# Optimization experiments

Hardware: AMD Instinct MI355X
Metric: run time of the kernel (lower is better)

The kernel has to match this reference:

```python
import jax, jax.numpy as jnp
import numpy as np

N_NODES = 100000
N_EDGES = 1600000
D = 128
N_LAYERS = 3
N_CLASSES = 10
N_GRAPHS = 512
BN_EPS = 1e-5


def setup_inputs() -> dict:
    key = jax.random.key(0)
    ks = jax.random.split(key, 16)
    s = 1.0 / np.sqrt(D)
    x = jax.random.normal(ks[0], (N_NODES, D), dtype=jnp.float32)
    edge_index = jax.random.randint(ks[1], (2, N_EDGES), 0, N_NODES, dtype=jnp.int32)
    batch = jnp.sort(jax.random.randint(ks[2], (N_NODES,), 0, N_GRAPHS, dtype=jnp.int32))
    W1s = jax.random.uniform(ks[3], (N_LAYERS, D, D), jnp.float32, -s, s)
    b1s = jax.random.uniform(ks[4], (N_LAYERS, D), jnp.float32, -s, s)
    W2s = jax.random.uniform(ks[5], (N_LAYERS, D, D), jnp.float32, -s, s)
    b2s = jax.random.uniform(ks[6], (N_LAYERS, D), jnp.float32, -s, s)
    gammas = jnp.ones((N_LAYERS, D), jnp.float32)
    betas = jnp.zeros((N_LAYERS, D), jnp.float32)
    lin1_w = jax.random.uniform(ks[7], (D, D), jnp.float32, -s, s)
    lin1_b = jax.random.uniform(ks[8], (D,), jnp.float32, -s, s)
    lin2_w = jax.random.uniform(ks[9], (D, N_CLASSES), jnp.float32, -s, s)
    lin2_b = jax.random.uniform(ks[10], (N_CLASSES,), jnp.float32, -s, s)
    return dict(x=x, edge_index=edge_index, batch=batch, W1s=W1s, b1s=b1s,
                W2s=W2s, b2s=b2s, gammas=gammas, betas=betas,
                lin1_w=lin1_w, lin1_b=lin1_b, lin2_w=lin2_w, lin2_b=lin2_b)


def _gin_layer(x, src, dst, W1, b1, W2, b2, gamma, beta):
    # scatter-add neighbor aggregation: sum_{j->i} x_j   (eps = 0)
    agg = jax.ops.segment_sum(x[src], dst, num_segments=N_NODES)
    h = x + agg
    h = jax.nn.relu(h @ W1 + b1)
    h = jax.nn.relu(h @ W2 + b2)
    # BatchNorm1d, training-mode batch stats (biased variance)
    mu = jnp.mean(h, axis=0)
    var = jnp.var(h, axis=0)
    return gamma * (h - mu) * jax.lax.rsqrt(var + BN_EPS) + beta


def reference(x, edge_index, batch, W1s, b1s, W2s, b2s, gammas, betas,
              lin1_w, lin1_b, lin2_w, lin2_b):
    src, dst = edge_index[0], edge_index[1]
    for l in range(N_LAYERS):
        x = _gin_layer(x, src, dst, W1s[l], b1s[l], W2s[l], b2s[l], gammas[l], betas[l])
    # global mean pool over graphs
    sums = jax.ops.segment_sum(x, batch, num_segments=N_GRAPHS)
    counts = jax.ops.segment_sum(jnp.ones((x.shape[0],), x.dtype), batch, num_segments=N_GRAPHS)
    pooled = sums / jnp.maximum(counts, 1.0)[:, None]
    h = jax.nn.relu(pooled @ lin1_w + lin1_b)  # dropout = identity (eval)
    return h @ lin2_w + lin2_b
```

## Files before the change

### kernel.cpp

```cpp
#include <hip/hip_runtime.h>
#include <hip/hip_bf16.h>

#define N_NODES 100000
#define N_EDGES 1600000
#define DD 128
#define N_GRAPHS 512
#define BN_EPS 1e-5f
#define NTILES 3125
#define SCAN_B 98
#define RED_B 25
#define PART_N 12500

typedef unsigned int u32;
typedef unsigned char u8;
typedef __bf16 bf16_t;
typedef __bf16 bf16x2 __attribute__((ext_vector_type(2)));
typedef __bf16 bf16x4 __attribute__((ext_vector_type(4)));
typedef __bf16 bf16x8 __attribute__((ext_vector_type(8)));
typedef float f32x4 __attribute__((ext_vector_type(4)));

__device__ __forceinline__ float bflo2f(u32 u) {
    union { u32 i; float f; } x; x.i = u << 16; return x.f;
}
__device__ __forceinline__ float bfhi2f(u32 u) {
    union { u32 i; float f; } x; x.i = u & 0xffff0000u; return x.f;
}
__device__ __forceinline__ u32 pack4u(float v0, float v1, float v2, float v3, float inv) {
    u32 q0 = (u32)fminf(rintf(v0 * inv), 255.f);
    u32 q1 = (u32)fminf(rintf(v1 * inv), 255.f);
    u32 q2 = (u32)fminf(rintf(v2 * inv), 255.f);
    u32 q3 = (u32)fminf(rintf(v3 * inv), 255.f);
    return q0 | (q1 << 8) | (q2 << 16) | (q3 << 24);
}


__global__ void k_zero(float4* p, int n) {
    float4 z = make_float4(0.f, 0.f, 0.f, 0.f);
    for (int i = blockIdx.x * blockDim.x + threadIdx.x; i < n; i += gridDim.x * blockDim.x)
        p[i] = z;
}

__global__ void k_hist8(const int* __restrict__ dst, int* __restrict__ deg) {
    const int part = blockIdx.x & 7;
    const int lo = part * PART_N, hi = lo + PART_N;
    const int start = (blockIdx.x >> 3) * blockDim.x + threadIdx.x;
    const int stride = (gridDim.x >> 3) * blockDim.x;
    for (int e = start; e < N_EDGES; e += stride) {
        int d = dst[e];
        if (d >= lo && d < hi) atomicAdd(&deg[d], 1);
    }
}

__global__ void k_scan1(const int* __restrict__ deg, int* __restrict__ bsum) {
    __shared__ int sh[1024];
    int b = blockIdx.x, t = threadIdx.x;
    int i = b * 1024 + t;
    int pd = (i < N_NODES) ? ((deg[i] + 3) & ~3) : 0;
    sh[t] = pd;
    __syncthreads();
    for (int s = 512; s > 0; s >>= 1) {
        if (t < s) sh[t] += sh[t + s];
        __syncthreads();
    }
    if (t == 0) bsum[b] = sh[0];
}
__global__ void k_scan2(const int* __restrict__ bsum, int* __restrict__ bbase,
                        int* __restrict__ poffs) {
    __shared__ int sh[128];
    int t = threadIdx.x;
    int v = (t < SCAN_B) ? bsum[t] : 0;
    sh[t] = v;
    __syncthreads();
    for (int d = 1; d < 128; d <<= 1) {
        int o = (t >= d) ? sh[t - d] : 0;
        __syncthreads();
        sh[t] += o;
        __syncthreads();
    }
    if (t < SCAN_B) bbase[t] = sh[t] - v;
    if (t == SCAN_B - 1) poffs[N_NODES] = sh[t];
}
__global__ void k_scan3(const int* __restrict__ deg, const int* __restrict__ bbase,
                        int* __restrict__ poffs, int* __restrict__ cursor) {
    __shared__ int sh[1024];
    int b = blockIdx.x, t = threadIdx.x;
    int i = b * 1024 + t;
    int pd = (i < N_NODES) ? ((deg[i] + 3) & ~3) : 0;
    sh[t] = pd;
    __syncthreads();
    for (int d = 1; d < 1024; d <<= 1) {
        int o = (t >= d) ? sh[t - d] : 0;
        __syncthreads();
        sh[t] += o;
        __syncthreads();
    }
    if (i < N_NODES) {
        int off = bbase[b] + sh[t] - pd;
        poffs[i] = off; cursor[i] = off;
    }
}

__global__ void k_fill8(const int* __restrict__ src, const int* __restrict__ dst,
                        int* __restrict__ cursor, int* __restrict__ csr) {
    const int part = blockIdx.x & 7;
    const int lo = part * PART_N, hi = lo + PART_N;
    const int start = (blockIdx.x >> 3) * blockDim.x + threadIdx.x;
    const int stride = (gridDim.x >> 3) * blockDim.x;
    for (int e = start; e < N_EDGES; e += stride) {
        int d = dst[e];
        if (d >= lo && d < hi) {
            int pos = atomicAdd(&cursor[d], 1);
            csr[pos] = src[e];
        }
    }
}

__global__ void k_pad(const int* __restrict__ deg, const int* __restrict__ poffs,
                      int* __restrict__ csr) {
    int t = blockIdx.x * blockDim.x + threadIdx.x;
    if (t >= N_NODES * 4) return;
    int n = t >> 2, j = t & 3;
    int s = poffs[n] + deg[n];
    if (s + j < poffs[n + 1]) csr[s + j] = n;
}

__global__ void k_cvt(const float* __restrict__ x, bf16_t* __restrict__ xb) {
    const int n4 = N_NODES * DD / 4;
    const float4* x4 = (const float4*)x;
    bf16x4* o4 = (bf16x4*)xb;
    for (int i = blockIdx.x * blockDim.x + threadIdx.x; i < n4; i += gridDim.x * blockDim.x) {
        float4 v = x4[i];
        bf16x4 o;
        o.x = (bf16_t)v.x; o.y = (bf16_t)v.y; o.z = (bf16_t)v.z; o.w = (bf16_t)v.w;
        o4[i] = o;
    }
}

__global__ void k_shufw(const float* __restrict__ W1s, const float* __restrict__ W2s,
                        bf16_t* __restrict__ wshuf) {
    int t = blockIdx.x * blockDim.x + threadIdx.x;
    if (t >= 6 * 16384) return;
    int g  = t >> 14;
    int r  = t & 16383;
    int j  = r & 7;
    int L  = (r >> 3) & 63;
    int nt = (r >> 9) & 7;
    int ks = r >> 12;
    int l  = g >> 1;
    const float* src = (g & 1) ? (W2s + l * 16384) : (W1s + l * 16384);
    int k = ks * 32 + (L >> 4) * 8 + j;
    int n = nt * 16 + (L & 15);
    wshuf[t] = (bf16_t)src[k * DD + n];
}

__global__ void k_aff_init(float* __restrict__ ss) {
    int f = threadIdx.x;
    if (f < DD) { ss[f] = 1.0f; ss[DD + f] = 0.0f; }
}

__global__ void k_red(const float* __restrict__ pstats, float* __restrict__ red) {
    int b = blockIdx.x;
    int t = threadIdx.x;
    const float* p = pstats + (size_t)b * 125 * 256 + t;
    float acc = 0.f;
    for (int i = 0; i < 125; ++i) acc += p[i * 256];
    red[b * 256 + t] = acc;
}

__global__ void k_aff_update(const float* __restrict__ red, const float* __restrict__ gamma,
                             const float* __restrict__ beta, float* __restrict__ scale,
                             float* __restrict__ shift) {
    int f = threadIdx.x;
    if (f < DD) {
        float s = 0.f, q = 0.f;
        for (int i = 0; i < RED_B; ++i) {
            s += red[i * 256 + f];
            q += red[i * 256 + 128 + f];
        }
        float mu  = s * (1.0f / N_NODES);
        float var = q * (1.0f / N_NODES) - mu * mu;
        float inv = rsqrtf(var + BN_EPS);
        float sc  = gamma[f] * inv;
        scale[f] = sc;
        shift[f] = beta[f] - mu * sc;
    }
}

__global__ void k_gbounds(const int* __restrict__ batch, int* __restrict__ gstart) {
    int i = blockIdx.x * blockDim.x + threadIdx.x;
    if (i >= N_NODES) return;
    int b = batch[i];
    int bp = (i == 0) ? -1 : batch[i - 1];
    for (int g = bp + 1; g <= b; ++g) gstart[g] = i;
    if (i == N_NODES - 1)
        for (int g = b + 1; g <= N_GRAPHS; ++g) gstart[g] = N_NODES;
}


template<bool IN_U8>
__device__ __forceinline__ void load_row8(
    const u8* __restrict__ xg, int r, int l16, float (&v)[8])
{
    if (IN_U8) {
        uint2 d = *(const uint2*)(xg + ((size_t)r << 7) + (l16 << 3));
        v[0] = (float)(d.x & 0xffu);
        v[1] = (float)((d.x >> 8) & 0xffu);
        v[2] = (float)((d.x >> 16) & 0xffu);
        v[3] = (float)(d.x >> 24);
        v[4] = (float)(d.y & 0xffu);
        v[5] = (float)((d.y >> 8) & 0xffu);
        v[6] = (float)((d.y >> 16) & 0xffu);
        v[7] = (float)(d.y >> 24);
    } else {
        uint4 d = *(const uint4*)(xg + ((size_t)r << 8) + (l16 << 4));
        v[0] = bflo2f(d.x); v[1] = bfhi2f(d.x);
        v[2] = bflo2f(d.y); v[3] = bfhi2f(d.y);
        v[4] = bflo2f(d.z); v[5] = bfhi2f(d.z);
        v[6] = bflo2f(d.w); v[7] = bfhi2f(d.w);
    }
}

template<bool IN_U8>
__device__ __forceinline__ void acc_group(
    const u8* __restrict__ xg, const float* __restrict__ xsc,
    int r, int l16, float (&a)[8])
{
    float v[8];
    load_row8<IN_U8>(xg, r, l16, v);
    if (IN_U8) {
        float s = xsc[r];
#pragma unroll
        for (int j = 0; j < 8; ++j) a[j] += s * v[j];
    } else {
#pragma unroll
        for (int j = 0; j < 8; ++j) a[j] += v[j];
    }
}

template<bool IN_U8>
__global__ __launch_bounds__(128, 8) void k_gather(
    const bf16_t* __restrict__ xb,
    const u8* __restrict__ x8, const float* __restrict__ xsc,
    const int* __restrict__ poffs, const int* __restrict__ csr,
    const int* __restrict__ deg,
    const float* __restrict__ scale, const float* __restrict__ shift,
    bf16_t* __restrict__ xt)
{
    const int tid  = threadIdx.x;
    const int w    = tid >> 6;
    const int lane = tid & 63;
    const int base = blockIdx.x * 32;
    const int q4   = lane >> 4;
    const int l16  = lane & 15;

    const u8* xg = IN_U8 ? x8 : (const u8*)xb;

    for (int rp = 0; rp < 8; ++rp) {
        const int rowA = (w << 4) + rp;
        const int rowB = rowA + 8;
        const int nA = base + rowA;
        const int nB = base + rowB;

        float aA[8] = {0.f, 0.f, 0.f, 0.f, 0.f, 0.f, 0.f, 0.f};
        float aB[8] = {0.f, 0.f, 0.f, 0.f, 0.f, 0.f, 0.f, 0.f};

        int eA = poffs[nA], eEA = poffs[nA + 1];
        int eB = poffs[nB], eEB = poffs[nB + 1];

        int rA = csr[eA + q4];
        int rB = csr[eB + q4];

        while ((eA < eEA) & (eB < eEB)) {
            int rA2 = csr[eA + 4 + q4];
            int rB2 = csr[eB + 4 + q4];
            acc_group<IN_U8>(xg, xsc, rA, l16, aA);
            acc_group<IN_U8>(xg, xsc, rB, l16, aB);
            rA = rA2; rB = rB2; eA += 4; eB += 4;
        }
        while (eA < eEA) {
            acc_group<IN_U8>(xg, xsc, rA, l16, aA);
            eA += 4; rA = csr[eA + q4];
        }
        while (eB < eEB) {
            acc_group<IN_U8>(xg, xsc, rB, l16, aB);
            eB += 4; rB = csr[eB + q4];
        }

        const int dgA = deg[nA], dgB = deg[nB];
        const float scoA = 1.f - (float)(((dgA + 3) & ~3) - dgA);
        const float scoB = 1.f - (float)(((dgB + 3) & ~3) - dgB);
        {
            int rs = (q4 & 1) ? nB : nA;
            float v[8];
            load_row8<IN_U8>(xg, rs, l16, v);
            float coA = (q4 == 0) ? scoA : 0.f;
            float coB = (q4 == 1) ? scoB : 0.f;
            if (IN_U8) {
                float s = xsc[rs];
                coA *= s; coB *= s;
            }
#pragma unroll
            for (int j = 0; j < 8; ++j) {
                aA[j] += coA * v[j];
                aB[j] += coB * v[j];
            }
        }

#pragma unroll
        for (int j = 0; j < 8; ++j) {
            aA[j] += __shfl_xor(aA[j], 16);
            aA[j] += __shfl_xor(aA[j], 32);
            aB[j] += __shfl_xor(aB[j], 16);
            aB[j] += __shfl_xor(aB[j], 32);
        }

        if (q4 < 2) {
            const bool selA = (q4 == 0);
            const float4 s0 = *(const float4*)(scale + (l16 << 3));
            const float4 s1 = *(const float4*)(scale + (l16 << 3) + 4);
            const float4 t0 = *(const float4*)(shift + (l16 << 3));
            const float4 t1 = *(const float4*)(shift + (l16 << 3) + 4);
            const float sarr[8] = {s0.x, s0.y, s0.z, s0.w, s1.x, s1.y, s1.z, s1.w};
            const float tarr[8] = {t0.x, t0.y, t0.z, t0.w, t1.x, t1.y, t1.z, t1.w};
            const int   node = selA ? nA : nB;
            const float cnt = (float)((selA ? dgA : dgB) + 1);
            bf16x8 pk;
#pragma unroll
            for (int j = 0; j < 8; ++j) {
                float av = selA ? aA[j] : aB[j];
                pk[j] = (bf16_t)(av * sarr[j] + cnt * tarr[j]);
            }
            *(bf16x8*)(xt + (size_t)node * DD + (l16 << 3)) = pk;
        }
    }
}

__global__ __launch_bounds__(128, 8) void k_mlp(
    const bf16_t* __restrict__ xt,
    u8* __restrict__ y8, float* __restrict__ ysc,
    const bf16_t* __restrict__ w1s, const bf16_t* __restrict__ w2s,
    const float* __restrict__ b1, const float* __restrict__ b2,
    float* __restrict__ pstats)
{
    __shared__ __align__(16) bf16_t tile[32 * 136];
    __shared__ float swsum[2][128];
    __shared__ float swsq[2][128];

    const int tid  = threadIdx.x;
    const int w    = tid >> 6;
    const int lane = tid & 63;
    const int base = blockIdx.x * 32;

    const int q = lane >> 4;
    const int c16 = lane & 15;
    const int arow = (w << 4) + c16;

    bf16x8 afr[4];
#pragma unroll
    for (int ks = 0; ks < 4; ++ks)
        afr[ks] = *(const bf16x8*)(xt + (size_t)(base + arow) * DD + ks * 32 + q * 8);

    f32x4 acc[8];
#pragma unroll
    for (int nt = 0; nt < 8; ++nt) acc[nt] = (f32x4){0.f, 0.f, 0.f, 0.f};
#pragma unroll
    for (int ks = 0; ks < 4; ++ks) {
#pragma unroll
        for (int nt = 0; nt < 8; ++nt) {
            bf16x8 bfr = *(const bf16x8*)(w1s + (((ks << 3) + nt) * 64 + lane) * 8);
            acc[nt] = __builtin_amdgcn_mfma_f32_16x16x32_bf16(afr[ks], bfr, acc[nt], 0, 0, 0);
        }
    }
#pragma unroll
    for (int nt = 0; nt < 8; ++nt) {
        float bias = b1[(nt << 4) + c16];
#pragma unroll
        for (int i = 0; i < 4; ++i) {
            float v = fmaxf(acc[nt][i] + bias, 0.f);
            int row = (w << 4) + (q << 2) + i;
            tile[row * 136 + (nt << 4) + c16] = (bf16_t)v;
        }
    }
    __syncthreads();

    bf16x8 afr2[4];
#pragma unroll
    for (int ks = 0; ks < 4; ++ks)
        afr2[ks] = *(const bf16x8*)(&tile[arow * 136 + ks * 32 + q * 8]);
    __syncthreads();

#pragma unroll
    for (int nt = 0; nt < 8; ++nt) acc[nt] = (f32x4){0.f, 0.f, 0.f, 0.f};
#pragma unroll
    for (int ks = 0; ks < 4; ++ks) {
#pragma unroll
        for (int nt = 0; nt < 8; ++nt) {
            bf16x8 bfr = *(const bf16x8*)(w2s + (((ks << 3) + nt) * 64 + lane) * 8);
            acc[nt] = __builtin_amdgcn_mfma_f32_16x16x32_bf16(afr2[ks], bfr, acc[nt], 0, 0, 0);
        }
    }
#pragma unroll
    for (int nt = 0; nt < 8; ++nt) {
        float bias = b2[(nt << 4) + c16];
        float s1 = 0.f, s2 = 0.f;
#pragma unroll
        for (int i = 0; i < 4; ++i) {
            float v = fmaxf(acc[nt][i] + bias, 0.f);
            int row = (w << 4) + (q << 2) + i;
            s1 += v;
            s2 += v * v;
            tile[row * 136 + (nt << 4) + c16] = (bf16_t)v;
        }
        s1 += __shfl_down(s1, 32); s2 += __shfl_down(s2, 32);
        s1 += __shfl_down(s1, 16); s2 += __shfl_down(s2, 16);
        if (lane < 16) {
            swsum[w][(nt << 4) + lane] = s1;
            swsq[w][(nt << 4) + lane] = s2;
        }
    }
    __syncthreads();

    {
        float ps = swsum[0][tid & 127] + swsum[1][tid & 127];
        float pq = swsq[0][tid & 127] + swsq[1][tid & 127];
        float* pb = pstats + (size_t)blockIdx.x * 256;
        pb[tid] = ps;
        pb[128 + tid] = pq;
    }

    {
        int row4 = tid >> 2, t4 = tid & 3;
        int node = base + row4;
        const bf16_t* tp = tile + row4 * 136 + t4 * 32;
        bf16x8 v0 = *(const bf16x8*)(tp);
        bf16x8 v1 = *(const bf16x8*)(tp + 8);
        bf16x8 v2 = *(const bf16x8*)(tp + 16);
        bf16x8 v3 = *(const bf16x8*)(tp + 24);
        float am = 0.f;
#pragma unroll
        for (int k = 0; k < 8; ++k) {
            am = fmaxf(am, (float)v0[k]);
            am = fmaxf(am, (float)v1[k]);
            am = fmaxf(am, (float)v2[k]);
            am = fmaxf(am, (float)v3[k]);
        }
        am = fmaxf(am, __shfl_xor(am, 1));
        am = fmaxf(am, __shfl_xor(am, 2));
        float inv = am > 0.f ? 255.f / am : 0.f;
        if (t4 == 0) ysc[node] = am * (1.f / 255.f);
        u32 u[8];
        u[0] = pack4u((float)v0[0], (float)v0[1], (float)v0[2], (float)v0[3], inv);
        u[1] = pack4u((float)v0[4], (float)v0[5], (float)v0[6], (float)v0[7], inv);
        u[2] = pack4u((float)v1[0], (float)v1[1], (float)v1[2], (float)v1[3], inv);
        u[3] = pack4u((float)v1[4], (float)v1[5], (float)v1[6], (float)v1[7], inv);
        u[4] = pack4u((float)v2[0], (float)v2[1], (float)v2[2], (float)v2[3], inv);
        u[5] = pack4u((float)v2[4], (float)v2[5], (float)v2[6], (float)v2[7], inv);
        u[6] = pack4u((float)v3[0], (float)v3[1], (float)v3[2], (float)v3[3], inv);
        u[7] = pack4u((float)v3[4], (float)v3[5], (float)v3[6], (float)v3[7], inv);
        uint4* yp = (uint4*)(y8 + (size_t)node * DD + t4 * 32);
        yp[0] = make_uint4(u[0], u[1], u[2], u[3]);
        yp[1] = make_uint4(u[4], u[5], u[6], u[7]);
    }
}


__global__ __launch_bounds__(256) void k_pool2u(
    const u8* __restrict__ y8, const float* __restrict__ ysc,
    const int* __restrict__ gstart,
    const float* __restrict__ scale, const float* __restrict__ shift,
    float* __restrict__ pooled)
{
    __shared__ float part[128];
    int g = blockIdx.x;
    int t = threadIdx.x;
    int f = t & 127, h = t >> 7;
    int s = gstart[g], e = gstart[g + 1];
    float acc = 0.f;
    for (int n = s + h; n < e; n += 2)
        acc += ysc[n] * (float)y8[(size_t)n * DD + f];
    if (h == 1) part[f] = acc;
    __syncthreads();
    if (h == 0) {
        acc += part[f];
        float cnt = (float)(e - s);
        float v = acc * scale[f] + cnt * shift[f];
        pooled[g * DD + f] = v / fmaxf(cnt, 1.0f);
    }
}

__global__ void k_head(const float* __restrict__ pooled,
                       const float* __restrict__ lin1w, const float* __restrict__ lin1b,
                       const float* __restrict__ lin2w, const float* __restrict__ lin2b,
                       float* __restrict__ out) {
    __shared__ float p[DD];
    __shared__ float h[DD];
    int g = blockIdx.x;
    int t = threadIdx.x;
    p[t] = pooled[g * DD + t];
    __syncthreads();
    float a = lin1b[t];
    for (int k = 0; k < DD; ++k) a += p[k] * lin1w[k * DD + t];
    h[t] = fmaxf(a, 0.f);
    __syncthreads();
    if (t < 10) {
        float o = lin2b[t];
        for (int k = 0; k < DD; ++k) o += h[k] * lin2w[k * 10 + t];
        out[g * 10 + t] = o;
    }
}


extern "C" void kernel_launch(void* const* d_in, const int* in_sizes, int n_in,
                              void* d_out, int out_size, void* d_ws, size_t ws_size,
                              hipStream_t stream) {
    const float* x      = (const float*)d_in[0];
    const int*   ei     = (const int*)d_in[1];
    const int*   batch  = (const int*)d_in[2];
    const float* W1s    = (const float*)d_in[3];
    const float* b1s    = (const float*)d_in[4];
    const float* W2s    = (const float*)d_in[5];
    const float* b2s    = (const float*)d_in[6];
    const float* gammas = (const float*)d_in[7];
    const float* betas  = (const float*)d_in[8];
    const float* lin1w  = (const float*)d_in[9];
    const float* lin1b  = (const float*)d_in[10];
    const float* lin2w  = (const float*)d_in[11];
    const float* lin2b  = (const float*)d_in[12];
    float* out = (float*)d_out;

    char* p = (char*)d_ws;
    size_t off = 0;
    auto alloc = [&](size_t bytes) -> char* {
        char* r = p + off;
        off += (bytes + 255) & ~(size_t)255;
        return r;
    };
    int*    deg    = (int*)alloc(N_NODES * 4);
    size_t zero_bytes = off;
    int*    poffs  = (int*)alloc((N_NODES + 1) * 4);
    int*    cursor = (int*)alloc(N_NODES * 4);
    int*    bsum   = (int*)alloc(128 * 4);
    int*    bbase  = (int*)alloc(128 * 4);
    int*    csr    = (int*)alloc(((size_t)N_EDGES + 4 * N_NODES + 64) * 4);
    bf16_t* xb     = (bf16_t*)alloc((size_t)N_NODES * DD * 2);
    u8*     q8a    = (u8*)alloc((size_t)N_NODES * DD);
    float*  sca    = (float*)alloc(N_NODES * 4);
    float*  scb    = (float*)alloc(N_NODES * 4);
    bf16_t* wshuf  = (bf16_t*)alloc(6 * 16384 * 2);
    float*  ss     = (float*)alloc(4 * 256 * 4);
    int*    gstart = (int*)alloc((N_GRAPHS + 1) * 4);
    float*  pooled = (float*)alloc(N_GRAPHS * DD * 4);
    bf16_t* xt     = (bf16_t*)alloc((size_t)N_NODES * DD * 2);
    float*  pstats = (float*)alloc((size_t)NTILES * 256 * 4);
    float*  red    = (float*)alloc(RED_B * 256 * 4);
    if (off > ws_size) return;

    u8* q8b = (u8*)xb;

    const int* srcA = ei;
    const int* dstA = ei + N_EDGES;

    k_zero<<<256, 256, 0, stream>>>((float4*)d_ws, (int)(zero_bytes / 16));
    k_hist8<<<1024, 256, 0, stream>>>(dstA, deg);
    k_scan1<<<SCAN_B, 1024, 0, stream>>>(deg, bsum);
    k_scan2<<<1, 128, 0, stream>>>(bsum, bbase, poffs);
    k_scan3<<<SCAN_B, 1024, 0, stream>>>(deg, bbase, poffs, cursor);
    k_fill8<<<1024, 256, 0, stream>>>(srcA, dstA, cursor, csr);
    k_pad<<<(N_NODES * 4 + 255) / 256, 256, 0, stream>>>(deg, poffs, csr);
    k_cvt<<<1024, 256, 0, stream>>>(x, xb);
    k_shufw<<<(6 * 16384 + 255) / 256, 256, 0, stream>>>(W1s, W2s, wshuf);
    k_aff_init<<<1, 128, 0, stream>>>(ss);
    k_gbounds<<<(N_NODES + 255) / 256, 256, 0, stream>>>(batch, gstart);

    k_gather<false><<<NTILES, 128, 0, stream>>>(
        xb, q8a, sca, poffs, csr, deg,
        ss + 0 * 256, ss + 0 * 256 + 128, xt);
    k_mlp<<<NTILES, 128, 0, stream>>>(
        xt, q8a, sca,
        wshuf + 0 * 16384, wshuf + 1 * 16384,
        b1s + 0 * DD, b2s + 0 * DD, pstats);
    k_red<<<RED_B, 256, 0, stream>>>(pstats, red);
    k_aff_update<<<1, 128, 0, stream>>>(red, gammas + 0 * DD, betas + 0 * DD,
                                        ss + 1 * 256, ss + 1 * 256 + 128);

    k_gather<true><<<NTILES, 128, 0, stream>>>(
        xb, q8a, sca, poffs, csr, deg,
        ss + 1 * 256, ss + 1 * 256 + 128, xt);
    k_mlp<<<NTILES, 128, 0, stream>>>(
        xt, q8b, scb,
        wshuf + 2 * 16384, wshuf + 3 * 16384,
        b1s + 1 * DD, b2s + 1 * DD, pstats);
    k_red<<<RED_B, 256, 0, stream>>>(pstats, red);
    k_aff_update<<<1, 128, 0, stream>>>(red, gammas + 1 * DD, betas + 1 * DD,
                                        ss + 2 * 256, ss + 2 * 256 + 128);

    k_gather<true><<<NTILES, 128, 0, stream>>>(
        xb, q8b, scb, poffs, csr, deg,
        ss + 2 * 256, ss + 2 * 256 + 128, xt);
    k_mlp<<<NTILES, 128, 0, stream>>>(
        xt, q8a, sca,
        wshuf + 4 * 16384, wshuf + 5 * 16384,
        b1s + 2 * DD, b2s + 2 * DD, pstats);
    k_red<<<RED_B, 256, 0, stream>>>(pstats, red);
    k_aff_update<<<1, 128, 0, stream>>>(red, gammas + 2 * DD, betas + 2 * DD,
                                        ss + 3 * 256, ss + 3 * 256 + 128);

    k_pool2u<<<N_GRAPHS, 256, 0, stream>>>(q8a, sca, gstart,
                                           ss + 3 * 256, ss + 3 * 256 + 128, pooled);
    k_head<<<N_GRAPHS, 128, 0, stream>>>(pooled, lin1w, lin1b, lin2w, lin2b, out);
}
```

Baseline: 611.1 us.

## Fuse neighbor gather and MLP into one per-layer kernel via LDS tile

Merges the gather and MLP kernels into a single `k_layer` kernel. The aggregated bf16 rows are staged in a shared-memory tile and fed straight to the MFMA matmuls, instead of going through a global `xt` buffer. This removes one full-size intermediate write and read per layer and one launch per layer. In exchange each block holds more shared memory and registers, and gets a serial gather-then-compute phase. The edge-index reads in the histogram and CSR-fill kernels also switch to nontemporal loads.

```diff
diff --git a/kernel.cpp b/kernel.cpp
--- a/kernel.cpp
+++ b/kernel.cpp
@@ -46,7 +46,7 @@
     const int start = (blockIdx.x >> 3) * blockDim.x + threadIdx.x;
     const int stride = (gridDim.x >> 3) * blockDim.x;
     for (int e = start; e < N_EDGES; e += stride) {
-        int d = dst[e];
+        int d = __builtin_nontemporal_load(dst + e);
         if (d >= lo && d < hi) atomicAdd(&deg[d], 1);
     }
 }
@@ -107,10 +107,11 @@
     const int start = (blockIdx.x >> 3) * blockDim.x + threadIdx.x;
     const int stride = (gridDim.x >> 3) * blockDim.x;
     for (int e = start; e < N_EDGES; e += stride) {
-        int d = dst[e];
+        int d = __builtin_nontemporal_load(dst + e);
         if (d >= lo && d < hi) {
+            int s = __builtin_nontemporal_load(src + e);
             int pos = atomicAdd(&cursor[d], 1);
-            csr[pos] = src[e];
+            csr[pos] = s;
         }
     }
 }
@@ -238,14 +239,21 @@
 }
 
 template<bool IN_U8>
-__global__ __launch_bounds__(128, 8) void k_gather(
+__global__ __launch_bounds__(128, 8) void k_layer(
     const bf16_t* __restrict__ xb,
     const u8* __restrict__ x8, const float* __restrict__ xsc,
+    u8* __restrict__ y8, float* __restrict__ ysc,
     const int* __restrict__ poffs, const int* __restrict__ csr,
     const int* __restrict__ deg,
     const float* __restrict__ scale, const float* __restrict__ shift,
-    bf16_t* __restrict__ xt)
+    const bf16_t* __restrict__ w1s, const bf16_t* __restrict__ w2s,
+    const float* __restrict__ b1, const float* __restrict__ b2,
+    float* __restrict__ pstats)
 {
+    __shared__ __align__(16) bf16_t tile[32 * 136];
+    __shared__ float swsum[2][128];
+    __shared__ float swsq[2][128];
+
     const int tid  = threadIdx.x;
     const int w    = tid >> 6;
     const int lane = tid & 63;
@@ -322,34 +330,18 @@
             const float4 t1 = *(const float4*)(shift + (l16 << 3) + 4);
             const float sarr[8] = {s0.x, s0.y, s0.z, s0.w, s1.x, s1.y, s1.z, s1.w};
             const float tarr[8] = {t0.x, t0.y, t0.z, t0.w, t1.x, t1.y, t1.z, t1.w};
-            const int   node = selA ? nA : nB;
             const float cnt = (float)((selA ? dgA : dgB) + 1);
+            const int   row = selA ? rowA : rowB;
             bf16x8 pk;
 #pragma unroll
             for (int j = 0; j < 8; ++j) {
                 float av = selA ? aA[j] : aB[j];
                 pk[j] = (bf16_t)(av * sarr[j] + cnt * tarr[j]);
             }
-            *(bf16x8*)(xt + (size_t)node * DD + (l16 << 3)) = pk;
-        }
-    }
-}
-
-__global__ __launch_bounds__(128, 8) void k_mlp(
-    const bf16_t* __restrict__ xt,
-    u8* __restrict__ y8, float* __restrict__ ysc,
-    const bf16_t* __restrict__ w1s, const bf16_t* __restrict__ w2s,
-    const float* __restrict__ b1, const float* __restrict__ b2,
-    float* __restrict__ pstats)
-{
-    __shared__ __align__(16) bf16_t tile[32 * 136];
-    __shared__ float swsum[2][128];
-    __shared__ float swsq[2][128];
-
-    const int tid  = threadIdx.x;
-    const int w    = tid >> 6;
-    const int lane = tid & 63;
-    const int base = blockIdx.x * 32;
+            *(bf16x8*)(&tile[row * 136 + (l16 << 3)]) = pk;
+        }
+    }
+    __syncthreads();
 
     const int q = lane >> 4;
     const int c16 = lane & 15;
@@ -358,7 +350,8 @@
     bf16x8 afr[4];
 #pragma unroll
     for (int ks = 0; ks < 4; ++ks)
-        afr[ks] = *(const bf16x8*)(xt + (size_t)(base + arow) * DD + ks * 32 + q * 8);
+        afr[ks] = *(const bf16x8*)(&tile[arow * 136 + ks * 32 + q * 8]);
+    __syncthreads();
 
     f32x4 acc[8];
 #pragma unroll
@@ -550,7 +543,6 @@
     float*  ss     = (float*)alloc(4 * 256 * 4);
     int*    gstart = (int*)alloc((N_GRAPHS + 1) * 4);
     float*  pooled = (float*)alloc(N_GRAPHS * DD * 4);
-    bf16_t* xt     = (bf16_t*)alloc((size_t)N_NODES * DD * 2);
     float*  pstats = (float*)alloc((size_t)NTILES * 256 * 4);
     float*  red    = (float*)alloc(RED_B * 256 * 4);
     if (off > ws_size) return;
@@ -572,33 +564,27 @@
     k_aff_init<<<1, 128, 0, stream>>>(ss);
     k_gbounds<<<(N_NODES + 255) / 256, 256, 0, stream>>>(batch, gstart);
 
-    k_gather<false><<<NTILES, 128, 0, stream>>>(
-        xb, q8a, sca, poffs, csr, deg,
-        ss + 0 * 256, ss + 0 * 256 + 128, xt);
-    k_mlp<<<NTILES, 128, 0, stream>>>(
-        xt, q8a, sca,
+    k_layer<false><<<NTILES, 128, 0, stream>>>(
+        xb, q8a, sca, q8a, sca, poffs, csr, deg,
+        ss + 0 * 256, ss + 0 * 256 + 128,
         wshuf + 0 * 16384, wshuf + 1 * 16384,
         b1s + 0 * DD, b2s + 0 * DD, pstats);
     k_red<<<RED_B, 256, 0, stream>>>(pstats, red);
     k_aff_update<<<1, 128, 0, stream>>>(red, gammas + 0 * DD, betas + 0 * DD,
                                         ss + 1 * 256, ss + 1 * 256 + 128);
 
-    k_gather<true><<<NTILES, 128, 0, stream>>>(
-        xb, q8a, sca, poffs, csr, deg,
-        ss + 1 * 256, ss + 1 * 256 + 128, xt);
-    k_mlp<<<NTILES, 128, 0, stream>>>(
-        xt, q8b, scb,
+    k_layer<true><<<NTILES, 128, 0, stream>>>(
+        xb, q8a, sca, q8b, scb, poffs, csr, deg,
+        ss + 1 * 256, ss + 1 * 256 + 128,
         wshuf + 2 * 16384, wshuf + 3 * 16384,
         b1s + 1 * DD, b2s + 1 * DD, pstats);
     k_red<<<RED_B, 256, 0, stream>>>(pstats, red);
     k_aff_update<<<1, 128, 0, stream>>>(red, gammas + 1 * DD, betas + 1 * DD,
                                         ss + 2 * 256, ss + 2 * 256 + 128);
 
-    k_gather<true><<<NTILES, 128, 0, stream>>>(
-        xb, q8b, scb, poffs, csr, deg,
-        ss + 2 * 256, ss + 2 * 256 + 128, xt);
-    k_mlp<<<NTILES, 128, 0, stream>>>(
-        xt, q8a, sca,
+    k_layer<true><<<NTILES, 128, 0, stream>>>(
+        xb, q8b, scb, q8a, sca, poffs, csr, deg,
+        ss + 2 * 256, ss + 2 * 256 + 128,
         wshuf + 4 * 16384, wshuf + 5 * 16384,
         b1s + 2 * DD, b2s + 2 * DD, pstats);
     k_red<<<RED_B, 256, 0, stream>>>(pstats, red);
```

After: 599.1 us. 1.02x faster.
